# Kernel tuning notes

Hardware: AMD Instinct MI355X
Metric: run time of the kernel (lower is better)

Reference implementation:

```python
import jax, jax.numpy as jnp
import numpy as np
from jax import lax

# QConv2d: conv2d implemented in the original via unfold + quantized matmul
# with a dequantization scale. High-precision path math:
#   out = scale * conv2d(x, weight) + bias
# We express the im2col+GEMM as the mathematically identical conv.

STRIDE = (1, 1)
PADDING = ((1, 1), (1, 1))


def setup_inputs() -> dict:
    key = jax.random.key(0)
    k1, k2, k3 = jax.random.split(key, 3)
    N, C, H, W = 16, 32, 256, 256
    O, KH, KW = 32, 3, 3
    x = jax.random.normal(k1, (N, C, H, W), dtype=jnp.float32)
    weight = jax.random.normal(k2, (O, C, KH, KW), dtype=jnp.float32) * 0.1
    bias = jax.random.normal(k3, (O,), dtype=jnp.float32)
    scale = jnp.float32(0.0078125)  # quantization dequant scale (1/128)
    return {"x": x, "weight": weight, "bias": bias, "scale": scale}


def reference(x, weight, bias, scale):
    # conv2d (NCHW / OIHW), stride 1, padding 1 -> same spatial size
    out = lax.conv_general_dilated(
        x, weight,
        window_strides=STRIDE,
        padding=PADDING,
        dimension_numbers=("NCHW", "OIHW", "NCHW"),
    )
    # scale applied by the quantized matmul kernel, then bias
    return out * scale + bias[None, :, None, None]
```

## Files before the change

### kernel.cpp

```cpp
#include <hip/hip_runtime.h>

typedef unsigned short u16;
typedef unsigned int   u32;
typedef short s8v  __attribute__((ext_vector_type(8)));
typedef float f16v __attribute__((ext_vector_type(16)));
typedef unsigned int u32x4 __attribute__((ext_vector_type(4)));

#define ROWBYTES 4224
#define NROWS    18
#define LDS_BYTES (NROWS * ROWBYTES)

__device__ inline u16 f2bf(float f) {
    u32 u = __builtin_bit_cast(u32, f);
    u += 0x7FFFu + ((u >> 16) & 1u);
    return (u16)(u >> 16);
}
__device__ inline u32 pk2(float lo, float hi) {
    return (u32)f2bf(lo) | ((u32)f2bf(hi) << 16);
}

__global__ __launch_bounds__(256, 2) void k_fused(const float* __restrict__ x,
                                                  const float* __restrict__ wgt,
                                                  const float* __restrict__ bias,
                                                  const float* __restrict__ scale_p,
                                                  float* __restrict__ out) {
    __shared__ __align__(16) char lds[LDS_BYTES];

    const int b    = ((blockIdx.x & 7) << 7) | (blockIdx.x >> 3);
    const int wb   = b & 3;
    const int hs   = (b >> 2) & 15;
    const int n    = b >> 6;
    const int w0   = wb << 6;
    const int h0   = hs << 4;
    const int t    = threadIdx.x;
    const int l    = t & 63;
    const int wave = t >> 6;
    const int g    = l >> 5;
    const int ln   = l & 31;

    {
        u16* wl = (u16*)lds;
        #pragma unroll
        for (int k = 0; k < 36; ++k) {
            const int idx = t + (k << 8);
            const int tap = idx % 9;
            const int oc  = idx / 9;
            wl[tap * 1024 + oc] = f2bf(wgt[idx]);
        }
    }
    __syncthreads();

    s8v A[9][2];
    {
        const u16* wl = (const u16*)lds;
        #pragma unroll
        for (int tap = 0; tap < 9; ++tap)
            #pragma unroll
            for (int q = 0; q < 2; ++q)
                A[tap][q] = *(const s8v*)(wl + tap * 1024 + ln * 32 + q * 16 + g * 8);
    }
    const float scale = scale_p[0];
    float bias_r[16];
    #pragma unroll
    for (int rg = 0; rg < 16; ++rg) bias_r[rg] = bias[(rg & 3) + 8 * (rg >> 2) + 4 * g];
    __syncthreads();

    const float* xbase = x + ((size_t)n << 21);

    if (t < 144) {
        const int cc   = t / 36;
        const int rem  = t - cc * 36;
        const int side = rem / 18;
        const int r    = rem - side * 18;
        const int hin  = h0 - 1 + r;
        const int wg   = w0 - 1 + side * 65;
        u32 q0 = 0, q1 = 0, q2 = 0, q3 = 0;
        if (hin >= 0 && hin < 256 && wg >= 0 && wg < 256) {
            const float* p = xbase + (size_t)(cc * 8) * 65536 + (size_t)hin * 256 + wg;
            q0 = pk2(p[0],      p[65536]);
            q1 = pk2(p[131072], p[196608]);
            q2 = pk2(p[262144], p[327680]);
            q3 = pk2(p[393216], p[458752]);
        }
        *(u32x4*)(lds + r * ROWBYTES + cc * 1056 + side * 1040) = u32x4{q0, q1, q2, q3};
    }

    {
        const float* pb = xbase + (size_t)(wave * 8) * 65536 + w0 + l;
        char* ldst = lds + wave * 1056 + ((l + 1) << 4);
        #pragma unroll
        for (int r = 0; r < NROWS; ++r) {
            const int hin = h0 - 1 + r;
            u32 q0 = 0, q1 = 0, q2 = 0, q3 = 0;
            if (hin >= 0 && hin < 256) {
                const float* p = pb + (size_t)hin * 256;
                const float c0 = p[0],      c1 = p[65536],  c2 = p[131072], c3 = p[196608];
                const float c4 = p[262144], c5 = p[327680], c6 = p[393216], c7 = p[458752];
                q0 = pk2(c0, c1); q1 = pk2(c2, c3); q2 = pk2(c4, c5); q3 = pk2(c6, c7);
            }
            *(u32x4*)(ldst + r * ROWBYTES) = u32x4{q0, q1, q2, q3};
        }
    }
    __syncthreads();

    #pragma unroll
    for (int i = 0; i < 4; ++i) {
        const int hr = (wave << 2) + i;

        f16v acc0, acc1;
        #pragma unroll
        for (int rg = 0; rg < 16; ++rg) { acc0[rg] = 0.f; acc1[rg] = 0.f; }

        #pragma unroll
        for (int kh = 0; kh < 3; ++kh) {
            const char* rowp = lds + (hr + kh) * ROWBYTES + g * 1056 + (ln << 4);
            #pragma unroll
            for (int kw = 0; kw < 3; ++kw) {
                const int tap = kh * 3 + kw;
                #pragma unroll
                for (int q = 0; q < 2; ++q) {
                    const char* pB = rowp + q * 2112 + (kw << 4);
                    const s8v b0 = *(const s8v*)pB;
                    const s8v b1 = *(const s8v*)(pB + 512);
                    acc0 = __builtin_amdgcn_mfma_f32_32x32x16_bf16(A[tap][q], b0, acc0, 0, 0, 0);
                    acc1 = __builtin_amdgcn_mfma_f32_32x32x16_bf16(A[tap][q], b1, acc1, 0, 0, 0);
                }
            }
        }

        const int h = h0 + hr;
        float* op = out + ((size_t)n << 21) + (size_t)h * 256 + w0 + ln;
        #pragma unroll
        for (int rg = 0; rg < 16; ++rg) {
            const int o = (rg & 3) + 8 * (rg >> 2) + 4 * g;
            op[(size_t)o * 65536]      = scale * acc0[rg] + bias_r[rg];
            op[(size_t)o * 65536 + 32] = scale * acc1[rg] + bias_r[rg];
        }
    }
}

extern "C" void kernel_launch(void* const* d_in, const int* in_sizes, int n_in,
                              void* d_out, int out_size, void* d_ws, size_t ws_size,
                              hipStream_t stream) {
    const float* x     = (const float*)d_in[0];
    const float* wgt   = (const float*)d_in[1];
    const float* bias  = (const float*)d_in[2];
    const float* scale = (const float*)d_in[3];
    float* out = (float*)d_out;
    k_fused<<<dim3(1024), dim3(256), 0, stream>>>(x, wgt, bias, scale, out);
}
```

Baseline: 58.08 us.

## Retile conv to full-width 4-row strips with swizzled LDS and vector loads

Each block now covers a 4-row by full 256-wide strip instead of a 16x64 tile, using 512 threads. Input loads become float4 per lane with clamped row indices, and the LDS layout uses an XOR swizzle on pixel slots to avoid bank conflicts. The aim is to cut the halo overhead (6 rows staged per 4 output rows, no width halos except the padding) and to get wider coalesced global reads. In exchange the vertical halo ratio gets worse (1.5x rows versus 1.125x), and only one 512-thread block fits per CU, which may reduce latency hiding.

Result: slower. 62.81 us (+8.1%).

```diff
diff --git a/kernel.cpp b/kernel.cpp
--- a/kernel.cpp
+++ b/kernel.cpp
@@ -5,10 +5,12 @@
 typedef short s8v  __attribute__((ext_vector_type(8)));
 typedef float f16v __attribute__((ext_vector_type(16)));
 typedef unsigned int u32x4 __attribute__((ext_vector_type(4)));
+typedef float f4 __attribute__((ext_vector_type(4)));
 
-#define ROWBYTES 4224
-#define NROWS    18
-#define LDS_BYTES (NROWS * ROWBYTES)
+#define CHUNKB 4128
+#define RB2    16512
+#define SROWS  6
+#define LDS_BYTES (SROWS * RB2)
 
 __device__ inline u16 f2bf(float f) {
     u32 u = __builtin_bit_cast(u32, f);
@@ -19,30 +21,25 @@
     return (u32)f2bf(lo) | ((u32)f2bf(hi) << 16);
 }
 
-__global__ __launch_bounds__(256, 2) void k_fused(const float* __restrict__ x,
+__global__ __launch_bounds__(512, 1) void k_fused(const float* __restrict__ x,
                                                   const float* __restrict__ wgt,
                                                   const float* __restrict__ bias,
                                                   const float* __restrict__ scale_p,
                                                   float* __restrict__ out) {
     __shared__ __align__(16) char lds[LDS_BYTES];
 
-    const int b    = ((blockIdx.x & 7) << 7) | (blockIdx.x >> 3);
-    const int wb   = b & 3;
-    const int hs   = (b >> 2) & 15;
-    const int n    = b >> 6;
-    const int w0   = wb << 6;
-    const int h0   = hs << 4;
-    const int t    = threadIdx.x;
-    const int l    = t & 63;
-    const int wave = t >> 6;
-    const int g    = l >> 5;
-    const int ln   = l & 31;
+    const int bid     = blockIdx.x;
+    const int logical = ((bid & 7) << 7) | (bid >> 3);
+    const int n  = logical >> 6;
+    const int hb = logical & 63;
+    const int h0 = hb << 2;
+    const int t = threadIdx.x, l = t & 63, wave = t >> 6, g = l >> 5, ln = l & 31;
 
     {
         u16* wl = (u16*)lds;
         #pragma unroll
-        for (int k = 0; k < 36; ++k) {
-            const int idx = t + (k << 8);
+        for (int k = 0; k < 18; ++k) {
+            const int idx = t + (k << 9);
             const int tap = idx % 9;
             const int oc  = idx / 9;
             wl[tap * 1024 + oc] = f2bf(wgt[idx]);
@@ -67,74 +64,79 @@
 
     const float* xbase = x + ((size_t)n << 21);
 
-    if (t < 144) {
-        const int cc   = t / 36;
-        const int rem  = t - cc * 36;
-        const int side = rem / 18;
-        const int r    = rem - side * 18;
-        const int hin  = h0 - 1 + r;
-        const int wg   = w0 - 1 + side * 65;
-        u32 q0 = 0, q1 = 0, q2 = 0, q3 = 0;
-        if (hin >= 0 && hin < 256 && wg >= 0 && wg < 256) {
-            const float* p = xbase + (size_t)(cc * 8) * 65536 + (size_t)hin * 256 + wg;
-            q0 = pk2(p[0],      p[65536]);
-            q1 = pk2(p[131072], p[196608]);
-            q2 = pk2(p[262144], p[327680]);
-            q3 = pk2(p[393216], p[458752]);
-        }
-        *(u32x4*)(lds + r * ROWBYTES + cc * 1056 + side * 1040) = u32x4{q0, q1, q2, q3};
+    if (t < 48) {
+        const int r = t >> 3, q = (t >> 1) & 3, side = t & 1;
+        *(u32x4*)(lds + r * RB2 + q * CHUNKB + (side ? 257 : 0) * 16) = u32x4{0, 0, 0, 0};
     }
 
     {
-        const float* pb = xbase + (size_t)(wave * 8) * 65536 + w0 + l;
-        char* ldst = lds + wave * 1056 + ((l + 1) << 4);
+        const int q  = wave & 3;
+        const int rs = wave >> 2;
+        const float* cb = xbase + (size_t)(q * 8) * 65536 + 4 * l;
         #pragma unroll
-        for (int r = 0; r < NROWS; ++r) {
-            const int hin = h0 - 1 + r;
-            u32 q0 = 0, q1 = 0, q2 = 0, q3 = 0;
-            if (hin >= 0 && hin < 256) {
-                const float* p = pb + (size_t)hin * 256;
-                const float c0 = p[0],      c1 = p[65536],  c2 = p[131072], c3 = p[196608];
-                const float c4 = p[262144], c5 = p[327680], c6 = p[393216], c7 = p[458752];
-                q0 = pk2(c0, c1); q1 = pk2(c2, c3); q2 = pk2(c4, c5); q3 = pk2(c6, c7);
+        for (int cp = 0; cp < 4; ++cp) {
+            const float* p0 = cb + (size_t)(2 * cp) * 65536;
+            const float* p1 = p0 + 65536;
+            f4 v0[3], v1[3];
+            int hcl[3], bad[3];
+            #pragma unroll
+            for (int ri = 0; ri < 3; ++ri) {
+                const int hin = h0 - 1 + rs + 2 * ri;
+                hcl[ri] = hin < 0 ? 0 : (hin > 255 ? 255 : hin);
+                bad[ri] = (hin < 0) | (hin > 255);
+                v0[ri] = *(const f4*)(p0 + (size_t)hcl[ri] * 256);
             }
-            *(u32x4*)(ldst + r * ROWBYTES) = u32x4{q0, q1, q2, q3};
+            #pragma unroll
+            for (int ri = 0; ri < 3; ++ri)
+                v1[ri] = *(const f4*)(p1 + (size_t)hcl[ri] * 256);
+            #pragma unroll
+            for (int ri = 0; ri < 3; ++ri) {
+                const int r = rs + 2 * ri;
+                char* rb = lds + r * RB2 + q * CHUNKB + cp * 4;
+                #pragma unroll
+                for (int i = 0; i < 4; ++i) {
+                    const int ps   = 4 * l + 1 + i;
+                    const int slot = ps ^ ((ps >> 4) & 7);
+                    const u32 pk = bad[ri] ? 0u : pk2(v0[ri][i], v1[ri][i]);
+                    *(u32*)(rb + slot * 16) = pk;
+                }
+            }
         }
     }
     __syncthreads();
 
+    const int hr = wave & 3;
+    const int ph = wave >> 2;
+    const int h  = h0 + hr;
     #pragma unroll
-    for (int i = 0; i < 4; ++i) {
-        const int hr = (wave << 2) + i;
+    for (int pn = 0; pn < 4; ++pn) {
+        const int px0 = ph * 128 + pn * 32;
 
-        f16v acc0, acc1;
+        f16v acc;
         #pragma unroll
-        for (int rg = 0; rg < 16; ++rg) { acc0[rg] = 0.f; acc1[rg] = 0.f; }
+        for (int rg = 0; rg < 16; ++rg) acc[rg] = 0.f;
 
         #pragma unroll
         for (int kh = 0; kh < 3; ++kh) {
-            const char* rowp = lds + (hr + kh) * ROWBYTES + g * 1056 + (ln << 4);
+            const char* rb = lds + (hr + kh) * RB2 + g * CHUNKB;
             #pragma unroll
             for (int kw = 0; kw < 3; ++kw) {
-                const int tap = kh * 3 + kw;
+                const int ps   = px0 + ln + kw;
+                const int slot = ps ^ ((ps >> 4) & 7);
+                const int tap  = kh * 3 + kw;
                 #pragma unroll
-                for (int q = 0; q < 2; ++q) {
-                    const char* pB = rowp + q * 2112 + (kw << 4);
-                    const s8v b0 = *(const s8v*)pB;
-                    const s8v b1 = *(const s8v*)(pB + 512);
-                    acc0 = __builtin_amdgcn_mfma_f32_32x32x16_bf16(A[tap][q], b0, acc0, 0, 0, 0);
-                    acc1 = __builtin_amdgcn_mfma_f32_32x32x16_bf16(A[tap][q], b1, acc1, 0, 0, 0);
+                for (int q2 = 0; q2 < 2; ++q2) {
+                    const s8v b = *(const s8v*)(rb + q2 * 2 * CHUNKB + slot * 16);
+                    acc = __builtin_amdgcn_mfma_f32_32x32x16_bf16(A[tap][q2], b, acc, 0, 0, 0);
                 }
             }
         }
 
-        const int h = h0 + hr;
-        float* op = out + ((size_t)n << 21) + (size_t)h * 256 + w0 + ln;
+        float* op = out + ((size_t)n << 21) + (size_t)h * 256 + px0 + ln;
         #pragma unroll
         for (int rg = 0; rg < 16; ++rg) {
             const int o = (rg & 3) + 8 * (rg >> 2) + 4 * g;
-            op[(size_t)o * 65536]      = scale * acc0[rg] + bias_r[rg];
-            op[(size_t)o * 65536 + 32] = scale * acc1[rg] + bias_r[rg];
+            op[(size_t)o * 65536] = scale * acc[rg] + bias_r[rg];
         }
     }
 }
@@ -147,5 +149,5 @@
     const float* bias  = (const float*)d_in[2];
     const float* scale = (const float*)d_in[3];
     float* out = (float*)d_out;
-    k_fused<<<dim3(1024), dim3(256), 0, stream>>>(x, wgt, bias, scale, out);
+    k_fused<<<dim3(1024), dim3(512), 0, stream>>>(x, wgt, bias, scale, out);
 }
```
